# Kernel optimization log

Measured on AMD Instinct MI355X. Metric: run time of the kernel, lower is better.

The kernel has to match this reference:

```python
import jax, jax.numpy as jnp
import numpy as np

B, L, D, H = 4, 2048, 512, 8
DH = D // H

def cdist(x):
    # torch.cdist(x, x) with p=2: (b,l,l) euclidean distances over feature dim
    sq = jnp.sum(x * x, axis=-1)  # (b,l)
    d2 = sq[:, :, None] + sq[:, None, :] - 2.0 * jnp.einsum('bld,bmd->blm', x, x)
    return jnp.sqrt(jnp.maximum(d2, 0.0))

def distance_residual_bias(cd, mask2d):
    # raw_max=True branch
    Dm = cd * mask2d
    row_max = jnp.max(Dm, axis=-1, keepdims=True)  # (b,l,1)
    Dm = row_max - Dm
    eye = jnp.eye(Dm.shape[-1], dtype=Dm.dtype)
    Dm = Dm * (1.0 - eye)  # zero diagonal
    return Dm * mask2d

def layernorm(x, g, b, eps=1e-5):
    mu = jnp.mean(x, axis=-1, keepdims=True)
    var = jnp.mean((x - mu) ** 2, axis=-1, keepdims=True)
    return (x - mu) * jax.lax.rsqrt(var + eps) * g + b

def setup_inputs() -> dict:
    key = jax.random.key(0)
    ks = jax.random.split(key, 16)
    s = lambda k, shape: jax.random.normal(k, shape, dtype=jnp.float32) * 0.02
    inp = {
        'x': jax.random.normal(ks[0], (B, L, D), dtype=jnp.float32),
        'node_mask': jnp.ones((B, L), dtype=jnp.float32),
        'wq': s(ks[1], (D, D)), 'bq': jnp.zeros((D,), jnp.float32),
        'wk': s(ks[2], (D, D)), 'bk': jnp.zeros((D,), jnp.float32),
        'wv': s(ks[3], (D, D)), 'bv': jnp.zeros((D,), jnp.float32),
        'wo': s(ks[4], (D, D)), 'bo': jnp.zeros((D,), jnp.float32),
        'ln1_g': jnp.ones((D,), jnp.float32), 'ln1_b': jnp.zeros((D,), jnp.float32),
        'w1': s(ks[5], (D, 4 * D)), 'b1': jnp.zeros((4 * D,), jnp.float32),
        'w2': s(ks[6], (4 * D, D)), 'b2': jnp.zeros((D,), jnp.float32),
        'ln2_g': jnp.ones((D,), jnp.float32), 'ln2_b': jnp.zeros((D,), jnp.float32),
    }
    return inp

def reference(x, node_mask, wq, bq, wk, bk, wv, bv, wo, bo,
              ln1_g, ln1_b, w1, b1, w2, b2, ln2_g, ln2_b):
    b, l, d = x.shape
    mask2d = node_mask[:, :, None] * node_mask[:, None, :]  # (b,l,l)
    bias = distance_residual_bias(cdist(x), mask2d)          # (b,l,l)

    q = (x @ wq + bq).reshape(b, l, H, DH).transpose(0, 2, 1, 3)
    k = (x @ wk + bk).reshape(b, l, H, DH).transpose(0, 2, 1, 3)
    v = (x @ wv + bv).reshape(b, l, H, DH).transpose(0, 2, 1, 3)
    scores = jnp.einsum('bhqd,bhkd->bhqk', q, k) / jnp.sqrt(jnp.float32(DH))
    scores = scores + bias[:, None, :, :]  # broadcast distance bias over heads
    attn = jax.nn.softmax(scores, axis=-1)
    y = jnp.einsum('bhqk,bhkd->bhqd', attn, v).transpose(0, 2, 1, 3).reshape(b, l, d)
    y = y @ wo + bo

    X = layernorm(x + y, ln1_g, ln1_b)            # AddNorm 1 (dropout=eval/no-op)
    ffn = jax.nn.relu(X @ w1 + b1) @ w2 + b2      # PositionWiseFFN
    X = layernorm(X + ffn, ln2_g, ln2_b)          # AddNorm 2
    return X
```

## Files before the change

kernel.cpp:

```cpp
#include <hip/hip_runtime.h>
#include <stdint.h>

#define GAS __attribute__((address_space(1)))
#define LAS __attribute__((address_space(3)))

typedef __attribute__((ext_vector_type(8))) __bf16 bf16x8;
typedef __attribute__((ext_vector_type(4))) float f32x4;

static constexpr int Bb = 4, Ll = 2048, Dd = 512, Hh = 8, DHd = 64;
static constexpr float LOG2E = 1.4426950408889634f;

__device__ __forceinline__ unsigned short f2bf(float f){
  unsigned u = __float_as_uint(f);
  u += 0x7fffu + ((u >> 16) & 1u);
  return (unsigned short)(u >> 16);
}
__device__ __forceinline__ void gload16(const void* g, void* l){
  __builtin_amdgcn_global_load_lds((const GAS void*)g, (LAS void*)l, 16, 0, 0);
}
__device__ __forceinline__ f32x4 mfma16(bf16x8 a, bf16x8 b, f32x4 c){
  return __builtin_amdgcn_mfma_f32_16x16x32_bf16(a, b, c, 0, 0, 0);
}
__device__ __forceinline__ float exp2_hw(float x){
  float r; asm("v_exp_f32 %0, %1" : "=v"(r) : "v"(x)); return r;
}

__global__ __launch_bounds__(256) void prep_all(
    const float* __restrict__ x,
    const float* __restrict__ wq, const float* __restrict__ wk,
    const float* __restrict__ wv, const float* __restrict__ wo,
    const float* __restrict__ w1, const float* __restrict__ w2,
    unsigned short* __restrict__ xbf, float* __restrict__ sq,
    unsigned short* __restrict__ wqkvT, unsigned short* __restrict__ woT,
    unsigned short* __restrict__ w1T, unsigned short* __restrict__ w2T)
{
  __shared__ float t[32][33];
  __shared__ float red[4];
  int bid = blockIdx.x;
  if (bid >= 3072){
    int row = bid - 3072, tid = threadIdx.x;
    float2 v = ((const float2*)(x + (size_t)row * Dd))[tid];
    ((unsigned*)(xbf + (size_t)row * Dd))[tid] =
        (unsigned)f2bf(v.x) | ((unsigned)f2bf(v.y) << 16);
    float s2 = v.x * v.x + v.y * v.y;
    #pragma unroll
    for (int s = 1; s < 64; s <<= 1) s2 += __shfl_xor(s2, s, 64);
    if ((tid & 63) == 0) red[tid >> 6] = s2;
    __syncthreads();
    if (tid == 0) sq[row] = red[0] + red[1] + red[2] + red[3];
    return;
  }
  const float* in; unsigned short* out; int R, C, bx, by;
  if (bid < 1024){
    int s = bid >> 8, tt = bid & 255;
    in  = s == 0 ? wq : s == 1 ? wk : s == 2 ? wv : wo;
    out = s == 3 ? woT : wqkvT + s * 512 * 512;
    R = 512; C = 512; bx = tt & 15; by = tt >> 4;
  } else if (bid < 2048){
    int tt = bid - 1024; in = w1; out = w1T; R = 512; C = 2048; bx = tt & 63; by = tt >> 6;
  } else {
    int tt = bid - 2048; in = w2; out = w2T; R = 2048; C = 512; bx = tt & 15; by = tt >> 4;
  }
  int tx = threadIdx.x & 31, ty = threadIdx.x >> 5;
  int c0 = bx * 32, r0 = by * 32;
  #pragma unroll
  for (int j = 0; j < 32; j += 8) t[ty + j][tx] = in[(size_t)(r0 + ty + j) * C + c0 + tx];
  __syncthreads();
  #pragma unroll
  for (int j = 0; j < 32; j += 8) out[(size_t)(c0 + ty + j) * R + r0 + tx] = f2bf(t[tx][ty + j]);
}

__global__ __launch_bounds__(256) void v_transpose(const unsigned short* __restrict__ qkv,
                                                   unsigned short* __restrict__ vT){
  int b = blockIdx.z, h = blockIdx.y, l0 = blockIdx.x * 64;
  int tid = threadIdx.x;
  __shared__ unsigned short t[64 * 64];
  #pragma unroll
  for (int it = 0; it < 2; ++it){
    int row = tid >> 2;
    int c = (tid & 3) + it * 4;
    uint4 d = *(const uint4*)(qkv + (size_t)(b * Ll + l0 + row) * 1536 + 1024 + h * DHd + c * 8);
    *(uint4*)((char*)t + row * 128 + ((c ^ (row & 7)) << 4)) = d;
  }
  __syncthreads();
  #pragma unroll
  for (int it = 0; it < 2; ++it){
    int dh = tid >> 2;
    int c2 = (tid & 3) + it * 4;
    unsigned pk[4];
    #pragma unroll
    for (int p = 0; p < 4; ++p){
      unsigned short e0, e1;
      {
        int ll = c2 * 8 + p * 2;
        e0 = *(const unsigned short*)((const char*)t + ll * 128 +
              ((((dh >> 3) ^ (ll & 7))) << 4) + ((dh & 7) << 1));
        ll = c2 * 8 + p * 2 + 1;
        e1 = *(const unsigned short*)((const char*)t + ll * 128 +
              ((((dh >> 3) ^ (ll & 7))) << 4) + ((dh & 7) << 1));
      }
      pk[p] = (unsigned)e0 | ((unsigned)e1 << 16);
    }
    uint4 o; o.x = pk[0]; o.y = pk[1]; o.z = pk[2]; o.w = pk[3];
    *(uint4*)(vT + ((size_t)(b * Hh + h) * DHd + dh) * Ll + l0 + c2 * 8) = o;
  }
}

template<int MODE>
__global__ __launch_bounds__(256) void gemm_bt(
    const unsigned short* __restrict__ A,
    const unsigned short* __restrict__ Bt,
    int M, int N, int K,
    const float* __restrict__ bias,
    const float* __restrict__ extra,
    float* __restrict__ outf,
    unsigned short* __restrict__ outb,
    const float* __restrict__ sq,
    float* __restrict__ rmax,
    const float* __restrict__ mask,
    const float* __restrict__ bias_k,
    const float* __restrict__ bias_v)
{
  int m0, n0, bxx = 0, byy = 0;
  if (MODE == 0){
    int z = blockIdx.z;
    A    += (size_t)z * Ll * Dd;
    Bt    = A;
    outb += (size_t)z * Ll * Ll;
    sq += z * Ll; rmax += z * Ll; mask += z * Ll;
    int tt = blockIdx.x, byv = 0;
    while (tt >= 16 - byv){ tt -= 16 - byv; byv++; }
    byy = byv; bxx = byv + tt;
    m0 = byy * 128; n0 = bxx * 128;
  } else {
    m0 = blockIdx.y * 128; n0 = blockIdx.x * 128;
  }
  if (MODE == 6){
    int z = blockIdx.z;
    A    += (size_t)z * (K >> 1);
    Bt   += (size_t)z * (K >> 1);
    outf += (size_t)z * (size_t)M * N;
  }
  const int KL = (MODE == 6) ? (K >> 1) : K;
  const int tid = threadIdx.x, w = tid >> 6, l = tid & 63;
  const int wm = w >> 1, wn = w & 1;
  __shared__ unsigned short lA[2][128 * 64];
  __shared__ unsigned short lB[2][128 * 64];
  f32x4 acc[4][4];
  const f32x4 z4 = {0.f, 0.f, 0.f, 0.f};
  #pragma unroll
  for (int i = 0; i < 4; i++){
    #pragma unroll
    for (int j = 0; j < 4; j++) acc[i][j] = z4;
  }
  const int srow = w * 8 + (l >> 3);
  const int sc = l & 7;

  #pragma unroll
  for (int j = 0; j < 4; j++){
    int row = j * 32 + srow;
    gload16(A + (size_t)(m0 + row) * K + ((sc ^ (row & 7)) << 3),
            &lA[0][0] + j * 2048 + w * 512);
    gload16(Bt + (size_t)(n0 + row) * K + ((sc ^ (row & 7)) << 3),
            &lB[0][0] + j * 2048 + w * 512);
  }
  __syncthreads();

  int cur = 0;
  for (int k0 = 0; k0 < KL; k0 += 64, cur ^= 1){
    if (k0 + 64 < KL){
      #pragma unroll
      for (int j = 0; j < 4; j++){
        int row = j * 32 + srow;
        gload16(A + (size_t)(m0 + row) * K + k0 + 64 + ((sc ^ (row & 7)) << 3),
                &lA[cur ^ 1][0] + j * 2048 + w * 512);
        gload16(Bt + (size_t)(n0 + row) * K + k0 + 64 + ((sc ^ (row & 7)) << 3),
                &lB[cur ^ 1][0] + j * 2048 + w * 512);
      }
    }
    bf16x8 af[4][2], bv[4][2];
    #pragma unroll
    for (int kk = 0; kk < 2; kk++){
      #pragma unroll
      for (int f = 0; f < 4; f++){
        int ra = wm * 64 + f * 16 + (l & 15);
        af[f][kk] = *(const bf16x8*)((const char*)&lA[cur][0] + ra * 128 +
                      (((kk * 4 + (l >> 4)) ^ (ra & 7)) << 4));
        int rb = wn * 64 + f * 16 + (l & 15);
        bv[f][kk] = *(const bf16x8*)((const char*)&lB[cur][0] + rb * 128 +
                      (((kk * 4 + (l >> 4)) ^ (rb & 7)) << 4));
      }
    }
    #pragma unroll
    for (int mf = 0; mf < 4; mf++){
      #pragma unroll
      for (int nf = 0; nf < 4; nf++){
        #pragma unroll
        for (int kk = 0; kk < 2; kk++)
          acc[mf][nf] = mfma16(af[mf][kk], bv[nf][kk], acc[mf][nf]);
      }
    }
    __syncthreads();
  }

  if (MODE == 0){
    float sqc[4], mkc[4];
    #pragma unroll
    for (int nf = 0; nf < 4; nf++){
      int col = n0 + wn * 64 + nf * 16 + (l & 15);
      sqc[nf] = sq[col]; mkc[nf] = mask[col];
    }
    #pragma unroll
    for (int mf = 0; mf < 4; mf++){
      #pragma unroll
      for (int r = 0; r < 4; r++){
        int row = m0 + wm * 64 + mf * 16 + (l >> 4) * 4 + r;
        float sqi = sq[row], mi = mask[row];
        #pragma unroll
        for (int nf = 0; nf < 4; nf++){
          float d2 = sqi + sqc[nf] - 2.f * acc[mf][nf][r];
          acc[mf][nf][r] = sqrtf(fmaxf(d2, 0.f)) * (mi * mkc[nf]) * LOG2E + 8.f;
        }
      }
    }
    #pragma unroll
    for (int mf = 0; mf < 4; mf++){
      #pragma unroll
      for (int r = 0; r < 4; r++){
        int row = m0 + wm * 64 + mf * 16 + (l >> 4) * 4 + r;
        float rm = 0.f;
        #pragma unroll
        for (int nf = 0; nf < 4; nf++){
          int col = n0 + wn * 64 + nf * 16 + (l & 15);
          outb[(size_t)row * Ll + col] = f2bf(acc[mf][nf][r]);
          rm = fmaxf(rm, acc[mf][nf][r]);
        }
        #pragma unroll
        for (int t = 1; t < 16; t <<= 1) rm = fmaxf(rm, __shfl_xor(rm, t, 64));
        if ((l & 15) == 0) atomicMax((int*)(rmax + row), __float_as_int(rm));
      }
    }
    if (bxx != byy){
      #pragma unroll
      for (int nf = 0; nf < 4; nf++){
        int col = n0 + wn * 64 + nf * 16 + (l & 15);
        float cm = 0.f;
        #pragma unroll
        for (int mf = 0; mf < 4; mf++){
          uint2 pk2;
          pk2.x = (unsigned)f2bf(acc[mf][nf][0]) | ((unsigned)f2bf(acc[mf][nf][1]) << 16);
          pk2.y = (unsigned)f2bf(acc[mf][nf][2]) | ((unsigned)f2bf(acc[mf][nf][3]) << 16);
          int rowb = m0 + wm * 64 + mf * 16 + (l >> 4) * 4;
          *(uint2*)(outb + (size_t)col * Ll + rowb) = pk2;
          cm = fmaxf(cm, fmaxf(fmaxf(acc[mf][nf][0], acc[mf][nf][1]),
                               fmaxf(acc[mf][nf][2], acc[mf][nf][3])));
        }
        cm = fmaxf(cm, __shfl_xor(cm, 16, 64));
        cm = fmaxf(cm, __shfl_xor(cm, 32, 64));
        if ((l >> 4) == 0) atomicMax((int*)(rmax + col), __float_as_int(cm));
      }
    }
  } else {
    #pragma unroll
    for (int mf = 0; mf < 4; mf++){
      #pragma unroll
      for (int r = 0; r < 4; r++){
        int row = m0 + wm * 64 + mf * 16 + (l >> 4) * 4 + r;
        #pragma unroll
        for (int nf = 0; nf < 4; nf++){
          int col = n0 + wn * 64 + nf * 16 + (l & 15);
          if (MODE == 6){
            outf[(size_t)row * N + col] = acc[mf][nf][r];
          } else {
            float bval;
            if (MODE == 5){
              const float* bp = col < 512 ? bias : (col < 1024 ? bias_k : bias_v);
              bval = bp[col & 511];
            } else {
              bval = bias[col];
            }
            float v = acc[mf][nf][r] + bval;
            if (MODE == 3) outb[(size_t)row * N + col] = f2bf(fmaxf(v, 0.f));
            if (MODE == 5) outb[(size_t)row * N + col] = f2bf(v);
            if (MODE == 2)
              outf[(size_t)row * N + col] = v + extra[(size_t)row * N + col];
          }
        }
      }
    }
  }
}

__global__ __launch_bounds__(256, 4) void flash_attn(
    const unsigned short* __restrict__ qkv,
    const unsigned short* __restrict__ vT,
    const unsigned short* __restrict__ cdm,
    const float* __restrict__ rmax,
    unsigned short* __restrict__ y)
{
  const int b = blockIdx.z, h = blockIdx.y, q0 = blockIdx.x * 64;
  const int tid = threadIdx.x, w = tid >> 6, l = tid & 63;
  const int ql = l & 15, lg = l >> 4;
  __shared__ unsigned short QPs[64 * 64];
  __shared__ unsigned short Ks[2][64 * 64];
  __shared__ unsigned short Vs[2][64 * 64];

  const int srow = w * 8 + (l >> 3);
  const int sc = l & 7;
  const unsigned short* kbase = qkv + (size_t)b * Ll * 1536 + 512 + h * DHd;
  const unsigned short* vbase = vT + (size_t)(b * Hh + h) * DHd * Ll;

  #pragma unroll
  for (int j = 0; j < 2; j++){
    int row = j * 32 + srow;
    gload16(qkv + (size_t)(b * Ll + q0 + row) * 1536 + h * DHd + ((sc ^ (row & 7)) << 3),
            QPs + j * 2048 + w * 512);
    gload16(kbase + (size_t)row * 1536 + ((sc ^ (row & 7)) << 3),
            &Ks[0][0] + j * 2048 + w * 512);
    gload16(vbase + (size_t)row * Ll + ((sc ^ (row & 7)) << 3),
            &Vs[0][0] + j * 2048 + w * 512);
  }

  const int qg = q0 + w * 16 + ql;
  const float rmx8 = rmax[b * Ll + qg] - 8.f;
  const unsigned short* cdrow = cdm + (size_t)(b * Ll + qg) * Ll;

  uint2 cdn[4];
  #pragma unroll
  for (int nf = 0; nf < 4; nf++)
    cdn[nf] = *(const uint2*)(cdrow + nf * 16 + lg * 4);

  f32x4 o[4];
  const f32x4 z4 = {0.f, 0.f, 0.f, 0.f};
  #pragma unroll
  for (int nf = 0; nf < 4; nf++) o[nf] = z4;
  float lsum = 0.f;

  __syncthreads();

  bf16x8 qa[2];
  #pragma unroll
  for (int kk = 0; kk < 2; kk++){
    int ra = w * 16 + ql;
    qa[kk] = *(const bf16x8*)((const char*)QPs + ra * 128 +
               (((kk * 4 + lg) ^ (ql & 7)) << 4));
  }

  const int NT = Ll / 64;
  for (int t = 0; t < NT; ++t){
    const int k0 = t * 64;
    const int cur = t & 1;

    uint2 cdc[4];
    #pragma unroll
    for (int nf = 0; nf < 4; nf++) cdc[nf] = cdn[nf];

    if (t + 1 < NT){
      const int kn = k0 + 64;
      #pragma unroll
      for (int nf = 0; nf < 4; nf++)
        cdn[nf] = *(const uint2*)(cdrow + kn + nf * 16 + lg * 4);
      #pragma unroll
      for (int j = 0; j < 2; j++){
        int row = j * 32 + srow;
        gload16(kbase + (size_t)(kn + row) * 1536 + ((sc ^ (row & 7)) << 3),
                &Ks[cur ^ 1][0] + j * 2048 + w * 512);
        gload16(vbase + (size_t)row * Ll + kn + ((sc ^ (row & 7)) << 3),
                &Vs[cur ^ 1][0] + j * 2048 + w * 512);
      }
    }

    f32x4 s[4];
    __builtin_amdgcn_s_setprio(1);
    #pragma unroll
    for (int nf = 0; nf < 4; nf++){
      s[nf] = z4;
      #pragma unroll
      for (int kk = 0; kk < 2; kk++){
        int rb = nf * 16 + ql;
        bf16x8 kb = *(const bf16x8*)((const char*)Ks[cur] + rb * 128 +
                      (((kk * 4 + lg) ^ (ql & 7)) << 4));
        s[nf] = mfma16(kb, qa[kk], s[nf]);
      }
    }
    __builtin_amdgcn_s_setprio(0);

    float sv[16];
    #pragma unroll
    for (int nf = 0; nf < 4; nf++){
      float c0 = __uint_as_float(cdc[nf].x << 16);
      float c1 = __uint_as_float(cdc[nf].x & 0xffff0000u);
      float c2 = __uint_as_float(cdc[nf].y << 16);
      float c3 = __uint_as_float(cdc[nf].y & 0xffff0000u);
      sv[nf * 4 + 0] = fmaf(s[nf][0], 0.125f * LOG2E, -c0);
      sv[nf * 4 + 1] = fmaf(s[nf][1], 0.125f * LOG2E, -c1);
      sv[nf * 4 + 2] = fmaf(s[nf][2], 0.125f * LOG2E, -c2);
      sv[nf * 4 + 3] = fmaf(s[nf][3], 0.125f * LOG2E, -c3);
    }
    if (k0 == q0){
      #pragma unroll
      for (int nf = 0; nf < 4; nf++) if (nf == w){
        #pragma unroll
        for (int r = 0; r < 4; r++)
          if (lg * 4 + r == ql) sv[nf * 4 + r] -= rmx8;
      }
    }

    float p[16], ps = 0.f;
    #pragma unroll
    for (int i = 0; i < 16; i++){ p[i] = exp2_hw(sv[i]); ps += p[i]; }
    lsum += ps;

    #pragma unroll
    for (int nf = 0; nf < 4; nf++){
      unsigned d0, d1;
      asm("v_cvt_pk_bf16_f32 %0, %1, %2" : "=v"(d0) : "v"(p[nf*4+0]), "v"(p[nf*4+1]));
      asm("v_cvt_pk_bf16_f32 %0, %1, %2" : "=v"(d1) : "v"(p[nf*4+2]), "v"(p[nf*4+3]));
      uint2 pk2; pk2.x = d0; pk2.y = d1;
      *(uint2*)((char*)QPs + w * 2048 + ql * 128 +
                ((nf * 32 + lg * 8) ^ ((ql & 7) << 4))) = pk2;
    }

    bf16x8 pa[2];
    #pragma unroll
    for (int kk = 0; kk < 2; kk++)
      pa[kk] = *(const bf16x8*)((const char*)QPs + w * 2048 + ql * 128 +
                 ((((kk * 4 + lg)) ^ (ql & 7)) << 4));
    __builtin_amdgcn_s_setprio(1);
    #pragma unroll
    for (int nf = 0; nf < 4; nf++){
      #pragma unroll
      for (int kk = 0; kk < 2; kk++){
        int rv = nf * 16 + ql;
        bf16x8 vb = *(const bf16x8*)((const char*)Vs[cur] + rv * 128 +
                      (((kk * 4 + lg) ^ (ql & 7)) << 4));
        o[nf] = mfma16(pa[kk], vb, o[nf]);
      }
    }
    __builtin_amdgcn_s_setprio(0);
    __syncthreads();
  }

  float ltot = lsum;
  ltot += __shfl_xor(ltot, 16, 64);
  ltot += __shfl_xor(ltot, 32, 64);
  float lf[4];
  #pragma unroll
  for (int r = 0; r < 4; r++)
    lf[r] = __shfl(ltot, (l & 48) | (lg * 4 + r), 64);
  #pragma unroll
  for (int nf = 0; nf < 4; nf++){
    #pragma unroll
    for (int r = 0; r < 4; r++){
      int qo = q0 + w * 16 + lg * 4 + r;
      float v = o[nf][r] / lf[r];
      y[(size_t)(b * Ll + qo) * Dd + h * DHd + nf * 16 + ql] = f2bf(v);
    }
  }
}

__global__ __launch_bounds__(256) void ln_kernel(const float* __restrict__ in,
                                                 const float* __restrict__ g,
                                                 const float* __restrict__ bt,
                                                 unsigned short* __restrict__ outb){
  int row = blockIdx.x, tid = threadIdx.x;
  float2 v = ((const float2*)(in + (size_t)row * Dd))[tid];
  float s = v.x + v.y, s2 = v.x * v.x + v.y * v.y;
  #pragma unroll
  for (int t = 1; t < 64; t <<= 1){ s += __shfl_xor(s, t, 64); s2 += __shfl_xor(s2, t, 64); }
  __shared__ float red[8];
  if ((tid & 63) == 0){ red[tid >> 6] = s; red[4 + (tid >> 6)] = s2; }
  __syncthreads();
  float S  = red[0] + red[1] + red[2] + red[3];
  float S2 = red[4] + red[5] + red[6] + red[7];
  float mu = S * (1.f / 512.f);
  float var = fmaxf(S2 * (1.f / 512.f) - mu * mu, 0.f);
  float rs = rsqrtf(var + 1e-5f);
  int c = tid * 2;
  float o0 = (v.x - mu) * rs * g[c] + bt[c];
  float o1 = (v.y - mu) * rs * g[c + 1] + bt[c + 1];
  ((unsigned*)(outb + (size_t)row * Dd))[tid] =
      (unsigned)f2bf(o0) | ((unsigned)f2bf(o1) << 16);
}

__global__ __launch_bounds__(256) void ln2p_kernel(
    const float* __restrict__ p01,
    const float* __restrict__ bias,
    const unsigned short* __restrict__ extra,
    const float* __restrict__ g, const float* __restrict__ bt,
    float* __restrict__ outf)
{
  int row = blockIdx.x, tid = threadIdx.x;
  float2 a0 = ((const float2*)(p01 + (size_t)row * Dd))[tid];
  float2 a1 = ((const float2*)(p01 + (size_t)Bb * Ll * Dd + (size_t)row * Dd))[tid];
  unsigned ex = ((const unsigned*)(extra + (size_t)row * Dd))[tid];
  float ex0 = __uint_as_float(ex << 16);
  float ex1 = __uint_as_float(ex & 0xffff0000u);
  int c = tid * 2;
  float vx = a0.x + a1.x + bias[c]     + ex0;
  float vy = a0.y + a1.y + bias[c + 1] + ex1;
  float s = vx + vy, s2 = vx * vx + vy * vy;
  #pragma unroll
  for (int t = 1; t < 64; t <<= 1){ s += __shfl_xor(s, t, 64); s2 += __shfl_xor(s2, t, 64); }
  __shared__ float red[8];
  if ((tid & 63) == 0){ red[tid >> 6] = s; red[4 + (tid >> 6)] = s2; }
  __syncthreads();
  float S  = red[0] + red[1] + red[2] + red[3];
  float S2 = red[4] + red[5] + red[6] + red[7];
  float mu = S * (1.f / 512.f);
  float var = fmaxf(S2 * (1.f / 512.f) - mu * mu, 0.f);
  float rs = rsqrtf(var + 1e-5f);
  float o0 = (vx - mu) * rs * g[c] + bt[c];
  float o1 = (vy - mu) * rs * g[c + 1] + bt[c + 1];
  float2 ov; ov.x = o0; ov.y = o1;
  ((float2*)(outf + (size_t)row * Dd))[tid] = ov;
}

extern "C" void kernel_launch(void* const* d_in, const int* in_sizes, int n_in,
                              void* d_out, int out_size, void* d_ws, size_t ws_size,
                              hipStream_t stream){
  const float* x     = (const float*)d_in[0];
  const float* nmask = (const float*)d_in[1];
  const float* wq = (const float*)d_in[2];  const float* bq = (const float*)d_in[3];
  const float* wk = (const float*)d_in[4];  const float* bk = (const float*)d_in[5];
  const float* wv = (const float*)d_in[6];  const float* bv = (const float*)d_in[7];
  const float* wo = (const float*)d_in[8];  const float* bo = (const float*)d_in[9];
  const float* ln1g = (const float*)d_in[10]; const float* ln1b = (const float*)d_in[11];
  const float* w1 = (const float*)d_in[12]; const float* b1 = (const float*)d_in[13];
  const float* w2 = (const float*)d_in[14]; const float* b2 = (const float*)d_in[15];
  const float* ln2g = (const float*)d_in[16]; const float* ln2b = (const float*)d_in[17];
  float* outp = (float*)d_out;
  char* ws = (char*)d_ws;

  unsigned short* xbf   = (unsigned short*)(ws + 0);
  float* sq   = (float*)(ws + 8388608);
  float* rmax = (float*)(ws + 8421376);
  unsigned short* wqkvT = (unsigned short*)(ws + 8454144);
  unsigned short* woT   = (unsigned short*)(ws + 10027008);
  unsigned short* w1T   = (unsigned short*)(ws + 10551296);
  unsigned short* w2T   = (unsigned short*)(ws + 12648448);
  unsigned short* cdm   = (unsigned short*)(ws + 14745600);
  unsigned short* qkv   = (unsigned short*)(ws + 48300032);
  unsigned short* vT    = (unsigned short*)(ws + 73465856);
  unsigned short* yb    = (unsigned short*)(ws + 81854464);
  float* res = (float*)(ws + 90243072);
  float* p01 = res;
  unsigned short* h1  = cdm;
  unsigned short* Xbf = qkv;

  hipMemsetAsync(rmax, 0, sizeof(float) * Bb * Ll, stream);

  prep_all<<<3072 + Bb * Ll, 256, 0, stream>>>(x, wq, wk, wv, wo, w1, w2,
                                               xbf, sq, wqkvT, woT, w1T, w2T);

  gemm_bt<0><<<dim3(136, 1, 4), 256, 0, stream>>>(xbf, xbf, Ll, Ll, Dd,
      nullptr, nullptr, nullptr, cdm, sq, rmax, nmask, nullptr, nullptr);

  gemm_bt<5><<<dim3(12, 64, 1), 256, 0, stream>>>(xbf, wqkvT, Bb * Ll, 1536, Dd,
      bq, nullptr, nullptr, qkv, nullptr, nullptr, nullptr, bk, bv);

  v_transpose<<<dim3(Ll / 64, Hh, Bb), 256, 0, stream>>>(qkv, vT);

  flash_attn<<<dim3(Ll / 64, Hh, Bb), 256, 0, stream>>>(qkv, vT, cdm, rmax, yb);

  gemm_bt<2><<<dim3(4, 64, 1), 256, 0, stream>>>(yb, woT, Bb * Ll, Dd, Dd,
      bo, x, res, nullptr, nullptr, nullptr, nullptr, nullptr, nullptr);

  ln_kernel<<<Bb * Ll, 256, 0, stream>>>(res, ln1g, ln1b, Xbf);

  gemm_bt<3><<<dim3(16, 64, 1), 256, 0, stream>>>(Xbf, w1T, Bb * Ll, 4 * Dd, Dd,
      b1, nullptr, nullptr, h1, nullptr, nullptr, nullptr, nullptr, nullptr);
  gemm_bt<6><<<dim3(4, 64, 2), 256, 0, stream>>>(h1, w2T, Bb * Ll, Dd, 4 * Dd,
      nullptr, nullptr, p01, nullptr, nullptr, nullptr, nullptr, nullptr, nullptr);

  ln2p_kernel<<<Bb * Ll, 256, 0, stream>>>(p01, b2, Xbf, ln2g, ln2b, outp);
}
```

Measured before the change: 252.8 us.

## Merge cdist and QKV GEMMs into one launch; drop setprio in attention

Combines the per-batch cdist Gram GEMM (544 triangular tiles) and the QKV projection GEMM (768 tiles) into a single 1312-block kernel that branches on block index. This removes one launch and lets the two independent GEMMs fill the GPU together instead of leaving a tail after each. It also removes the s_setprio hints around the MFMA sections in flash attention, which may change how waves interleave. The generic gemm_bt template is trimmed to the remaining modes.

```diff
diff --git a/kernel.cpp b/kernel.cpp
--- a/kernel.cpp
+++ b/kernel.cpp
@@ -106,42 +106,33 @@
   }
 }
 
-template<int MODE>
-__global__ __launch_bounds__(256) void gemm_bt(
-    const unsigned short* __restrict__ A,
-    const unsigned short* __restrict__ Bt,
-    int M, int N, int K,
-    const float* __restrict__ bias,
-    const float* __restrict__ extra,
-    float* __restrict__ outf,
-    unsigned short* __restrict__ outb,
-    const float* __restrict__ sq,
-    float* __restrict__ rmax,
-    const float* __restrict__ mask,
-    const float* __restrict__ bias_k,
-    const float* __restrict__ bias_v)
+__global__ __launch_bounds__(256) void gemm_cq(
+    const unsigned short* __restrict__ xbf,
+    const unsigned short* __restrict__ wqkvT,
+    const float* __restrict__ bq, const float* __restrict__ bk,
+    const float* __restrict__ bv,
+    unsigned short* __restrict__ cdm, unsigned short* __restrict__ qkv,
+    const float* __restrict__ sq, float* __restrict__ rmax,
+    const float* __restrict__ mask)
 {
-  int m0, n0, bxx = 0, byy = 0;
-  if (MODE == 0){
-    int z = blockIdx.z;
-    A    += (size_t)z * Ll * Dd;
-    Bt    = A;
-    outb += (size_t)z * Ll * Ll;
-    sq += z * Ll; rmax += z * Ll; mask += z * Ll;
-    int tt = blockIdx.x, byv = 0;
+  const int bid = blockIdx.x;
+  const bool isc = bid < 544;
+  const unsigned short *Ap, *Bp;
+  int m0, n0, bxx = 0, byy = 0, zb = 0;
+  if (isc){
+    zb = bid >> 7;
+    zb = bid / 136;
+    int tt = bid - zb * 136, byv = 0;
     while (tt >= 16 - byv){ tt -= 16 - byv; byv++; }
     byy = byv; bxx = byv + tt;
     m0 = byy * 128; n0 = bxx * 128;
+    Ap = xbf + (size_t)zb * Ll * Dd; Bp = Ap;
   } else {
-    m0 = blockIdx.y * 128; n0 = blockIdx.x * 128;
-  }
-  if (MODE == 6){
-    int z = blockIdx.z;
-    A    += (size_t)z * (K >> 1);
-    Bt   += (size_t)z * (K >> 1);
-    outf += (size_t)z * (size_t)M * N;
-  }
-  const int KL = (MODE == 6) ? (K >> 1) : K;
+    int t = bid - 544;
+    int bx = t % 12, by = t / 12;
+    m0 = by * 128; n0 = bx * 128;
+    Ap = xbf; Bp = wqkvT;
+  }
   const int tid = threadIdx.x, w = tid >> 6, l = tid & 63;
   const int wm = w >> 1, wn = w & 1;
   __shared__ unsigned short lA[2][128 * 64];
@@ -159,26 +150,26 @@
   #pragma unroll
   for (int j = 0; j < 4; j++){
     int row = j * 32 + srow;
-    gload16(A + (size_t)(m0 + row) * K + ((sc ^ (row & 7)) << 3),
+    gload16(Ap + (size_t)(m0 + row) * Dd + ((sc ^ (row & 7)) << 3),
             &lA[0][0] + j * 2048 + w * 512);
-    gload16(Bt + (size_t)(n0 + row) * K + ((sc ^ (row & 7)) << 3),
+    gload16(Bp + (size_t)(n0 + row) * Dd + ((sc ^ (row & 7)) << 3),
             &lB[0][0] + j * 2048 + w * 512);
   }
   __syncthreads();
 
   int cur = 0;
-  for (int k0 = 0; k0 < KL; k0 += 64, cur ^= 1){
-    if (k0 + 64 < KL){
+  for (int k0 = 0; k0 < Dd; k0 += 64, cur ^= 1){
+    if (k0 + 64 < Dd){
       #pragma unroll
       for (int j = 0; j < 4; j++){
         int row = j * 32 + srow;
-        gload16(A + (size_t)(m0 + row) * K + k0 + 64 + ((sc ^ (row & 7)) << 3),
+        gload16(Ap + (size_t)(m0 + row) * Dd + k0 + 64 + ((sc ^ (row & 7)) << 3),
                 &lA[cur ^ 1][0] + j * 2048 + w * 512);
-        gload16(Bt + (size_t)(n0 + row) * K + k0 + 64 + ((sc ^ (row & 7)) << 3),
+        gload16(Bp + (size_t)(n0 + row) * Dd + k0 + 64 + ((sc ^ (row & 7)) << 3),
                 &lB[cur ^ 1][0] + j * 2048 + w * 512);
       }
     }
-    bf16x8 af[4][2], bv[4][2];
+    bf16x8 af[4][2], bvv[4][2];
     #pragma unroll
     for (int kk = 0; kk < 2; kk++){
       #pragma unroll
@@ -187,7 +178,7 @@
         af[f][kk] = *(const bf16x8*)((const char*)&lA[cur][0] + ra * 128 +
                       (((kk * 4 + (l >> 4)) ^ (ra & 7)) << 4));
         int rb = wn * 64 + f * 16 + (l & 15);
-        bv[f][kk] = *(const bf16x8*)((const char*)&lB[cur][0] + rb * 128 +
+        bvv[f][kk] = *(const bf16x8*)((const char*)&lB[cur][0] + rb * 128 +
                       (((kk * 4 + (l >> 4)) ^ (rb & 7)) << 4));
       }
     }
@@ -197,25 +188,29 @@
       for (int nf = 0; nf < 4; nf++){
         #pragma unroll
         for (int kk = 0; kk < 2; kk++)
-          acc[mf][nf] = mfma16(af[mf][kk], bv[nf][kk], acc[mf][nf]);
+          acc[mf][nf] = mfma16(af[mf][kk], bvv[nf][kk], acc[mf][nf]);
       }
     }
     __syncthreads();
   }
 
-  if (MODE == 0){
+  if (isc){
+    unsigned short* outb = cdm + (size_t)zb * Ll * Ll;
+    const float* sqz = sq + zb * Ll;
+    const float* mkz = mask + zb * Ll;
+    float* rmz = rmax + zb * Ll;
     float sqc[4], mkc[4];
     #pragma unroll
     for (int nf = 0; nf < 4; nf++){
       int col = n0 + wn * 64 + nf * 16 + (l & 15);
-      sqc[nf] = sq[col]; mkc[nf] = mask[col];
+      sqc[nf] = sqz[col]; mkc[nf] = mkz[col];
     }
     #pragma unroll
     for (int mf = 0; mf < 4; mf++){
       #pragma unroll
       for (int r = 0; r < 4; r++){
         int row = m0 + wm * 64 + mf * 16 + (l >> 4) * 4 + r;
-        float sqi = sq[row], mi = mask[row];
+        float sqi = sqz[row], mi = mkz[row];
         #pragma unroll
         for (int nf = 0; nf < 4; nf++){
           float d2 = sqi + sqc[nf] - 2.f * acc[mf][nf][r];
@@ -237,7 +232,7 @@
         }
         #pragma unroll
         for (int t = 1; t < 16; t <<= 1) rm = fmaxf(rm, __shfl_xor(rm, t, 64));
-        if ((l & 15) == 0) atomicMax((int*)(rmax + row), __float_as_int(rm));
+        if ((l & 15) == 0) atomicMax((int*)(rmz + row), __float_as_int(rm));
       }
     }
     if (bxx != byy){
@@ -257,7 +252,7 @@
         }
         cm = fmaxf(cm, __shfl_xor(cm, 16, 64));
         cm = fmaxf(cm, __shfl_xor(cm, 32, 64));
-        if ((l >> 4) == 0) atomicMax((int*)(rmax + col), __float_as_int(cm));
+        if ((l >> 4) == 0) atomicMax((int*)(rmz + col), __float_as_int(cm));
       }
     }
   } else {
@@ -269,22 +264,109 @@
         #pragma unroll
         for (int nf = 0; nf < 4; nf++){
           int col = n0 + wn * 64 + nf * 16 + (l & 15);
-          if (MODE == 6){
-            outf[(size_t)row * N + col] = acc[mf][nf][r];
-          } else {
-            float bval;
-            if (MODE == 5){
-              const float* bp = col < 512 ? bias : (col < 1024 ? bias_k : bias_v);
-              bval = bp[col & 511];
-            } else {
-              bval = bias[col];
-            }
-            float v = acc[mf][nf][r] + bval;
-            if (MODE == 3) outb[(size_t)row * N + col] = f2bf(fmaxf(v, 0.f));
-            if (MODE == 5) outb[(size_t)row * N + col] = f2bf(v);
-            if (MODE == 2)
-              outf[(size_t)row * N + col] = v + extra[(size_t)row * N + col];
-          }
+          const float* bp = col < 512 ? bq : (col < 1024 ? bk : bv);
+          float v = acc[mf][nf][r] + bp[col & 511];
+          qkv[(size_t)row * 1536 + col] = f2bf(v);
+        }
+      }
+    }
+  }
+}
+
+template<int MODE>
+__global__ __launch_bounds__(256) void gemm_bt(
+    const unsigned short* __restrict__ A,
+    const unsigned short* __restrict__ Bt,
+    int M, int N, int K,
+    const float* __restrict__ bias,
+    const float* __restrict__ extra,
+    float* __restrict__ outf,
+    unsigned short* __restrict__ outb)
+{
+  int m0 = blockIdx.y * 128, n0 = blockIdx.x * 128;
+  if (MODE == 6){
+    int z = blockIdx.z;
+    A    += (size_t)z * (K >> 1);
+    Bt   += (size_t)z * (K >> 1);
+    outf += (size_t)z * (size_t)M * N;
+  }
+  const int KL = (MODE == 6) ? (K >> 1) : K;
+  const int tid = threadIdx.x, w = tid >> 6, l = tid & 63;
+  const int wm = w >> 1, wn = w & 1;
+  __shared__ unsigned short lA[2][128 * 64];
+  __shared__ unsigned short lB[2][128 * 64];
+  f32x4 acc[4][4];
+  const f32x4 z4 = {0.f, 0.f, 0.f, 0.f};
+  #pragma unroll
+  for (int i = 0; i < 4; i++){
+    #pragma unroll
+    for (int j = 0; j < 4; j++) acc[i][j] = z4;
+  }
+  const int srow = w * 8 + (l >> 3);
+  const int sc = l & 7;
+
+  #pragma unroll
+  for (int j = 0; j < 4; j++){
+    int row = j * 32 + srow;
+    gload16(A + (size_t)(m0 + row) * K + ((sc ^ (row & 7)) << 3),
+            &lA[0][0] + j * 2048 + w * 512);
+    gload16(Bt + (size_t)(n0 + row) * K + ((sc ^ (row & 7)) << 3),
+            &lB[0][0] + j * 2048 + w * 512);
+  }
+  __syncthreads();
+
+  int cur = 0;
+  for (int k0 = 0; k0 < KL; k0 += 64, cur ^= 1){
+    if (k0 + 64 < KL){
+      #pragma unroll
+      for (int j = 0; j < 4; j++){
+        int row = j * 32 + srow;
+        gload16(A + (size_t)(m0 + row) * K + k0 + 64 + ((sc ^ (row & 7)) << 3),
+                &lA[cur ^ 1][0] + j * 2048 + w * 512);
+        gload16(Bt + (size_t)(n0 + row) * K + k0 + 64 + ((sc ^ (row & 7)) << 3),
+                &lB[cur ^ 1][0] + j * 2048 + w * 512);
+      }
+    }
+    bf16x8 af[4][2], bv[4][2];
+    #pragma unroll
+    for (int kk = 0; kk < 2; kk++){
+      #pragma unroll
+      for (int f = 0; f < 4; f++){
+        int ra = wm * 64 + f * 16 + (l & 15);
+        af[f][kk] = *(const bf16x8*)((const char*)&lA[cur][0] + ra * 128 +
+                      (((kk * 4 + (l >> 4)) ^ (ra & 7)) << 4));
+        int rb = wn * 64 + f * 16 + (l & 15);
+        bv[f][kk] = *(const bf16x8*)((const char*)&lB[cur][0] + rb * 128 +
+                      (((kk * 4 + (l >> 4)) ^ (rb & 7)) << 4));
+      }
+    }
+    #pragma unroll
+    for (int mf = 0; mf < 4; mf++){
+      #pragma unroll
+      for (int nf = 0; nf < 4; nf++){
+        #pragma unroll
+        for (int kk = 0; kk < 2; kk++)
+          acc[mf][nf] = mfma16(af[mf][kk], bv[nf][kk], acc[mf][nf]);
+      }
+    }
+    __syncthreads();
+  }
+
+  #pragma unroll
+  for (int mf = 0; mf < 4; mf++){
+    #pragma unroll
+    for (int r = 0; r < 4; r++){
+      int row = m0 + wm * 64 + mf * 16 + (l >> 4) * 4 + r;
+      #pragma unroll
+      for (int nf = 0; nf < 4; nf++){
+        int col = n0 + wn * 64 + nf * 16 + (l & 15);
+        if (MODE == 6){
+          outf[(size_t)row * N + col] = acc[mf][nf][r];
+        } else {
+          float v = acc[mf][nf][r] + bias[col];
+          if (MODE == 3) outb[(size_t)row * N + col] = f2bf(fmaxf(v, 0.f));
+          if (MODE == 2)
+            outf[(size_t)row * N + col] = v + extra[(size_t)row * N + col];
         }
       }
     }
@@ -371,7 +453,6 @@
     }
 
     f32x4 s[4];
-    __builtin_amdgcn_s_setprio(1);
     #pragma unroll
     for (int nf = 0; nf < 4; nf++){
       s[nf] = z4;
@@ -383,7 +464,6 @@
         s[nf] = mfma16(kb, qa[kk], s[nf]);
       }
     }
-    __builtin_amdgcn_s_setprio(0);
 
     float sv[16];
     #pragma unroll
@@ -426,7 +506,6 @@
     for (int kk = 0; kk < 2; kk++)
       pa[kk] = *(const bf16x8*)((const char*)QPs + w * 2048 + ql * 128 +
                  ((((kk * 4 + lg)) ^ (ql & 7)) << 4));
-    __builtin_amdgcn_s_setprio(1);
     #pragma unroll
     for (int nf = 0; nf < 4; nf++){
       #pragma unroll
@@ -437,7 +516,6 @@
         o[nf] = mfma16(pa[kk], vb, o[nf]);
       }
     }
-    __builtin_amdgcn_s_setprio(0);
     __syncthreads();
   }
 
@@ -553,25 +631,22 @@
   prep_all<<<3072 + Bb * Ll, 256, 0, stream>>>(x, wq, wk, wv, wo, w1, w2,
                                                xbf, sq, wqkvT, woT, w1T, w2T);
 
-  gemm_bt<0><<<dim3(136, 1, 4), 256, 0, stream>>>(xbf, xbf, Ll, Ll, Dd,
-      nullptr, nullptr, nullptr, cdm, sq, rmax, nmask, nullptr, nullptr);
-
-  gemm_bt<5><<<dim3(12, 64, 1), 256, 0, stream>>>(xbf, wqkvT, Bb * Ll, 1536, Dd,
-      bq, nullptr, nullptr, qkv, nullptr, nullptr, nullptr, bk, bv);
+  gemm_cq<<<1312, 256, 0, stream>>>(xbf, wqkvT, bq, bk, bv,
+                                    cdm, qkv, sq, rmax, nmask);
 
   v_transpose<<<dim3(Ll / 64, Hh, Bb), 256, 0, stream>>>(qkv, vT);
 
   flash_attn<<<dim3(Ll / 64, Hh, Bb), 256, 0, stream>>>(qkv, vT, cdm, rmax, yb);
 
   gemm_bt<2><<<dim3(4, 64, 1), 256, 0, stream>>>(yb, woT, Bb * Ll, Dd, Dd,
-      bo, x, res, nullptr, nullptr, nullptr, nullptr, nullptr, nullptr);
+      bo, x, res, nullptr);
 
   ln_kernel<<<Bb * Ll, 256, 0, stream>>>(res, ln1g, ln1b, Xbf);
 
   gemm_bt<3><<<dim3(16, 64, 1), 256, 0, stream>>>(Xbf, w1T, Bb * Ll, 4 * Dd, Dd,
-      b1, nullptr, nullptr, h1, nullptr, nullptr, nullptr, nullptr, nullptr);
+      b1, nullptr, nullptr, h1);
   gemm_bt<6><<<dim3(4, 64, 2), 256, 0, stream>>>(h1, w2T, Bb * Ll, Dd, 4 * Dd,
-      nullptr, nullptr, p01, nullptr, nullptr, nullptr, nullptr, nullptr, nullptr);
+      nullptr, nullptr, p01, nullptr);
 
   ln2p_kernel<<<Bb * Ll, 256, 0, stream>>>(p01, b2, Xbf, ln2g, ln2b, outp);
 }
```

After: 232.6 us. 1.09x faster.
